# Kernel tuning notes

Hardware: AMD Instinct MI355X
Metric: run time of the kernel (lower is better)

## Reference

```python
import jax, jax.numpy as jnp
import numpy as np

H, W = 256, 256
FRONT_K = 8
ALPHA_T = 1.0 / 255.0
EPS = 1e-8               # transmittance early-stop threshold (meta_f32[4])
BG = (0.0, 0.0, 0.0)     # background color
CHUNK = 128              # gaussians composited per scan step


def setup_inputs() -> dict:
    key = jax.random.key(0)
    k1, k2, k3, k4, k5, k6, k7 = jax.random.split(key, 7)
    B, G = 2, 8192
    # gaussian centers spread over the image plane
    means2d = jax.random.uniform(k1, (B, G, 2), jnp.float32) * jnp.array([W, H], jnp.float32)
    # positive-definite conics (inverse 2D covariance): a, c > 0, |b| < sqrt(a*c)
    a = 0.05 + 0.45 * jax.random.uniform(k2, (B, G), jnp.float32)
    c = 0.05 + 0.45 * jax.random.uniform(k3, (B, G), jnp.float32)
    b = 0.5 * (jax.random.uniform(k4, (B, G), jnp.float32) - 0.5) * jnp.sqrt(a * c)
    conics = jnp.stack([a, b, c], axis=-1)
    colors = jax.random.uniform(k5, (B, G, 3), jnp.float32)
    opacities = jax.random.uniform(k6, (B, G), jnp.float32)
    depths = jax.random.uniform(k7, (B, G), jnp.float32) * 10.0
    return {"means2d": means2d, "conics": conics, "colors": colors,
            "opacities": opacities, "depths": depths}


def _rasterize_one(means2d, conics, colors, opacities, depths):
    # depth sort (stable, front-to-back)
    perm = jnp.argsort(depths, stable=True)
    m = means2d[perm]      # [G,2]
    co = conics[perm]      # [G,3]
    col = colors[perm]     # [G,3]
    op = opacities[perm]   # [G]
    G = m.shape[0]
    n_chunks = G // CHUNK

    px = jnp.arange(W, dtype=jnp.float32) + 0.5  # pixel centers
    py = jnp.arange(H, dtype=jnp.float32) + 0.5
    bg = jnp.asarray(BG, jnp.float32)

    def step(carry, chunk):
        accum, T, count = carry                    # [H,W,3], [H,W], [H,W] int32
        mC, coC, colC, opC = chunk                 # [K,2],[K,3],[K,3],[K]
        dx = px[None, None, :] - mC[:, 0][:, None, None]   # [K,1,W]
        dy = py[None, :, None] - mC[:, 1][:, None, None]   # [K,H,1]
        a = coC[:, 0][:, None, None]
        b = coC[:, 1][:, None, None]
        c = coC[:, 2][:, None, None]
        sigma = 0.5 * (a * dx * dx + c * dy * dy) + b * dx * dy  # [K,H,W]
        alpha = jnp.minimum(opC[:, None, None] * jnp.exp(-sigma), 0.999)
        alpha = jnp.where((sigma >= 0.0) & (alpha >= ALPHA_T), alpha, 0.0)
        kept = (alpha > 0.0).astype(jnp.int32)
        # front_k: only the first FRONT_K contributing gaussians per pixel
        before = count[None] + jnp.cumsum(kept, axis=0) - kept
        alpha = jnp.where(before < FRONT_K, alpha, 0.0)
        kept = (alpha > 0.0).astype(jnp.int32)
        one_m = 1.0 - alpha
        cp = jnp.cumprod(one_m, axis=0)                              # [K,H,W]
        Tc = T[None] * jnp.concatenate([jnp.ones((1, H, W), alpha.dtype), cp[:-1]], 0)
        w = jnp.where(Tc > EPS, Tc * alpha, 0.0)                     # early-stop gate
        accum = accum + jnp.einsum('khw,kc->hwc', w, colC)
        T = T * cp[-1]
        count = count + jnp.sum(kept, axis=0)
        return (accum, T, count), None

    chunks = (m.reshape(n_chunks, CHUNK, 2),
              co.reshape(n_chunks, CHUNK, 3),
              col.reshape(n_chunks, CHUNK, 3),
              op.reshape(n_chunks, CHUNK))
    init = (jnp.zeros((H, W, 3), jnp.float32),
            jnp.ones((H, W), jnp.float32),
            jnp.zeros((H, W), jnp.int32))
    (accum, T, _), _ = jax.lax.scan(step, init, chunks)
    return accum + T[..., None] * bg


def reference(means2d, conics, colors, opacities, depths):
    return jax.vmap(_rasterize_one)(means2d, conics, colors, opacities, depths)
```

## Files before the change

### kernel.cpp

```cpp
#include <hip/hip_runtime.h>
#include <math.h>

#define GN 8192
#define BN 2
#define HN 256
#define WN 256
#define FRONT_K 8
#define EPS_T 1e-8f
#define ALPHA_T (1.0f / 255.0f)
#define TDIM 32
#define NTILE (TDIM * TDIM)
#define CAP 256

__global__ __launch_bounds__(64) void pgr_clear(unsigned* __restrict__ cur)
{
    cur[blockIdx.x * 64 + threadIdx.x] = 0u;
}

__global__ __launch_bounds__(64) void pgr_prep(
    const float* __restrict__ means2d, const float* __restrict__ conics,
    const float* __restrict__ colors, const float* __restrict__ opac,
    float4* __restrict__ dat0, float4* __restrict__ dat1,
    float* __restrict__ dat2, unsigned* __restrict__ cur,
    unsigned* __restrict__ ent)
{
    int g = blockIdx.x * 64 + threadIdx.x;
    int b = g >> 13, i = g & (GN - 1);
    float2 mxy = reinterpret_cast<const float2*>(means2d)[g];
    float mx = mxy.x, my = mxy.y;
    float ca = conics[3 * g], cb = conics[3 * g + 1], cc = conics[3 * g + 2];
    float r = colors[3 * g], g2 = colors[3 * g + 1], b3 = colors[3 * g + 2];
    float op = opac[g];

    dat0[g] = make_float4(mx, my, ca, cb);
    dat1[g] = make_float4(cc, op, r, g2);
    dat2[g] = b3;

    float s = (op > 0.f) ? (__logf(255.0f * op) + 1e-4f) : -1.0f;
    if (s < 0.f) return;
    float det = fmaxf(ca * cc - cb * cb, 1e-12f);
    float dxm = sqrtf(2.f * s * cc / det) + 0.02f;
    float dym = sqrtf(2.f * s * ca / det) + 0.02f;
    int x0 = (int)floorf(mx - dxm - 0.5f), x1 = (int)ceilf(mx + dxm - 0.5f);
    int y0 = (int)floorf(my - dym - 0.5f), y1 = (int)ceilf(my + dym - 0.5f);
    if (x1 < 0 || x0 > WN - 1 || y1 < 0 || y0 > HN - 1) return;
    x0 = max(x0, 0); x1 = min(x1, WN - 1);
    y0 = max(y0, 0); y1 = min(y1, HN - 1);
    int tx0 = x0 >> 3, tx1 = x1 >> 3, ty0 = y0 >> 3, ty1 = y1 >> 3;
    for (int ty = ty0; ty <= ty1; ++ty)
        for (int tx = tx0; tx <= tx1; ++tx) {
            int t = b * NTILE + ty * TDIM + tx;
            unsigned pos = atomicAdd(&cur[t], 1u);
            if (pos < CAP) ent[t * CAP + pos] = (unsigned)i;
        }
}

__device__ __forceinline__ int rank_of(const unsigned long long* s_key,
                                       unsigned long long k, int L)
{
    int rank = 0, j = 0;
    for (; j + 4 <= L; j += 4) {
        unsigned long long k0 = s_key[j], k1 = s_key[j + 1];
        unsigned long long k2 = s_key[j + 2], k3 = s_key[j + 3];
        rank += (int)(k0 < k) + (int)(k1 < k) + (int)(k2 < k) + (int)(k3 < k);
    }
    for (; j < L; ++j) rank += (int)(s_key[j] < k);
    return rank;
}

__global__ __launch_bounds__(64) void pgr_raster(
    const float* __restrict__ depths, const float4* __restrict__ dat0,
    const float4* __restrict__ dat1, const float* __restrict__ dat2,
    const unsigned* __restrict__ cur, const unsigned* __restrict__ ent,
    float* __restrict__ out)
{
    const int b = blockIdx.z;
    const int t = b * NTILE + blockIdx.y * TDIM + blockIdx.x;
    const int tid = threadIdx.x;
    const int tx0 = blockIdx.x * 8, ty0 = blockIdx.y * 8;
    const int lx = tid & 7, ly = tid >> 3;
    const float px = tx0 + lx + 0.5f, py = ty0 + ly + 0.5f;
    const int bG = b * GN;

    __shared__ unsigned long long s_key[CAP];
    __shared__ float4 s_d0[CAP], s_d1[CAP];
    __shared__ float s_d2[CAP];

    unsigned eRaw = ent[t * CAP + tid];
    int e = (int)(eRaw & (GN - 1));
    int q = bG + e;
    float myd = depths[q];
    float4 r0 = dat0[q];
    float4 r1 = dat1[q];
    float r2 = dat2[q];
    const int L = min((int)cur[t], CAP);

    unsigned long long myk =
        ((unsigned long long)__float_as_uint(myd) << 13) | (unsigned)e;
    if (tid < L) s_key[tid] = myk;
    for (int i = 64 + tid; i < L; i += 64) {
        int ei = (int)(ent[t * CAP + i] & (GN - 1));
        s_key[i] = ((unsigned long long)__float_as_uint(depths[bG + ei]) << 13)
                   | (unsigned)ei;
    }
    __syncthreads();

    if (tid < L) {
        int rank = rank_of(s_key, myk, L);
        s_d0[rank] = r0; s_d1[rank] = r1; s_d2[rank] = r2;
    }
    for (int i = 64 + tid; i < L; i += 64) {
        unsigned long long k = s_key[i];
        int rank = rank_of(s_key, k, L);
        int qq = bG + (int)(k & (GN - 1));
        s_d0[rank] = dat0[qq]; s_d1[rank] = dat1[qq]; s_d2[rank] = dat2[qq];
    }
    __syncthreads();

    float accR = 0.f, accG = 0.f, accB = 0.f, T = 1.f;
    int count = 0;
    bool done = false;

    for (int i0 = 0; i0 < L; i0 += 8) {
        if (__all((int)done)) break;
        float alpha[8], colR[8], colG[8], colB[8];
        bool valid[8];
        #pragma unroll
        for (int k = 0; k < 8; ++k) {
            int idx = i0 + k;
            bool act = (idx < L) && !done;
            int ii = act ? idx : i0;
            float4 d0 = s_d0[ii];
            float4 d1 = s_d1[ii];
            float dx = __fsub_rn(px, d0.x);
            float dy = __fsub_rn(py, d0.y);
            float t1 = __fmul_rn(__fmul_rn(d0.z, dx), dx);
            float t2 = __fmul_rn(__fmul_rn(d1.x, dy), dy);
            float sigma = __fadd_rn(__fmul_rn(0.5f, __fadd_rn(t1, t2)),
                                    __fmul_rn(__fmul_rn(d0.w, dx), dy));
            bool v = act && sigma >= 0.f && sigma <= 5.55f;
            float al = v ? fminf(__fmul_rn(d1.y, __expf(-sigma)), 0.999f) : 0.f;
            valid[k] = v && (al >= ALPHA_T);
            alpha[k] = al;
            colR[k] = d1.z; colG[k] = d1.w; colB[k] = s_d2[ii];
        }
        #pragma unroll
        for (int k = 0; k < 8; ++k) {
            if (valid[k] && !done) {
                float al = alpha[k];
                if (T > EPS_T) {
                    float w = __fmul_rn(T, al);
                    accR += w * colR[k];
                    accG += w * colG[k];
                    accB += w * colB[k];
                }
                T = __fmul_rn(T, __fsub_rn(1.f, al));
                count++;
                if (count >= FRONT_K || T <= EPS_T) done = true;
            }
        }
    }

    int o = ((b * HN + (ty0 + ly)) * WN + (tx0 + lx)) * 3;
    out[o] = accR;
    out[o + 1] = accG;
    out[o + 2] = accB;
}

extern "C" void kernel_launch(void* const* d_in, const int* in_sizes, int n_in,
                              void* d_out, int out_size, void* d_ws, size_t ws_size,
                              hipStream_t stream) {
    const float* means2d = (const float*)d_in[0];
    const float* conics  = (const float*)d_in[1];
    const float* colors  = (const float*)d_in[2];
    const float* opac    = (const float*)d_in[3];
    const float* depths  = (const float*)d_in[4];
    float* out = (float*)d_out;

    const int BG = BN * GN;
    float4*   dat0 = (float4*)d_ws;
    float4*   dat1 = dat0 + BG;
    float*    dat2 = (float*)(dat1 + BG);
    unsigned* cur  = (unsigned*)(dat2 + BG);
    unsigned* ent  = cur + BN * NTILE;

    pgr_clear<<<(BN * NTILE) / 64, 64, 0, stream>>>(cur);
    pgr_prep<<<BG / 64, 64, 0, stream>>>(means2d, conics, colors, opac,
                                         dat0, dat1, dat2, cur, ent);
    pgr_raster<<<dim3(TDIM, TDIM, BN), 64, 0, stream>>>(
        depths, dat0, dat1, dat2, cur, ent, out);
}
```

Measured before the change: 46.70 us.

## Scatter full gaussian records and sort keys into per-tile bins during prep

The prep kernel now writes the depth key and all gaussian attributes (float4 x2 plus blue) directly into each tile's bin slot, instead of writing only the index and storing attributes once per gaussian. The raster kernel then reads keys and records contiguously per tile, with no indirect gathers through the index into depths and the attribute arrays. The cost is much more write traffic in prep (about 40 bytes per tile overlap instead of 4) and a far larger workspace footprint.

```diff
diff --git a/kernel.cpp b/kernel.cpp
--- a/kernel.cpp
+++ b/kernel.cpp
@@ -20,9 +20,10 @@
 __global__ __launch_bounds__(64) void pgr_prep(
     const float* __restrict__ means2d, const float* __restrict__ conics,
     const float* __restrict__ colors, const float* __restrict__ opac,
-    float4* __restrict__ dat0, float4* __restrict__ dat1,
-    float* __restrict__ dat2, unsigned* __restrict__ cur,
-    unsigned* __restrict__ ent)
+    const float* __restrict__ depths,
+    unsigned* __restrict__ cur, unsigned long long* __restrict__ kent,
+    float4* __restrict__ recA, float4* __restrict__ recB,
+    float* __restrict__ recC)
 {
     int g = blockIdx.x * 64 + threadIdx.x;
     int b = g >> 13, i = g & (GN - 1);
@@ -31,10 +32,7 @@
     float ca = conics[3 * g], cb = conics[3 * g + 1], cc = conics[3 * g + 2];
     float r = colors[3 * g], g2 = colors[3 * g + 1], b3 = colors[3 * g + 2];
     float op = opac[g];
-
-    dat0[g] = make_float4(mx, my, ca, cb);
-    dat1[g] = make_float4(cc, op, r, g2);
-    dat2[g] = b3;
+    float dep = depths[g];
 
     float s = (op > 0.f) ? (__logf(255.0f * op) + 1e-4f) : -1.0f;
     if (s < 0.f) return;
@@ -47,11 +45,23 @@
     x0 = max(x0, 0); x1 = min(x1, WN - 1);
     y0 = max(y0, 0); y1 = min(y1, HN - 1);
     int tx0 = x0 >> 3, tx1 = x1 >> 3, ty0 = y0 >> 3, ty1 = y1 >> 3;
+
+    unsigned long long key =
+        ((unsigned long long)__float_as_uint(dep) << 13) | (unsigned)i;
+    float4 A = make_float4(mx, my, ca, cb);
+    float4 B = make_float4(cc, op, r, g2);
+
     for (int ty = ty0; ty <= ty1; ++ty)
         for (int tx = tx0; tx <= tx1; ++tx) {
             int t = b * NTILE + ty * TDIM + tx;
             unsigned pos = atomicAdd(&cur[t], 1u);
-            if (pos < CAP) ent[t * CAP + pos] = (unsigned)i;
+            if (pos < CAP) {
+                int sl = t * CAP + (int)pos;
+                kent[sl] = key;
+                recA[sl] = A;
+                recB[sl] = B;
+                recC[sl] = b3;
+            }
         }
 }
 
@@ -69,10 +79,9 @@
 }
 
 __global__ __launch_bounds__(64) void pgr_raster(
-    const float* __restrict__ depths, const float4* __restrict__ dat0,
-    const float4* __restrict__ dat1, const float* __restrict__ dat2,
-    const unsigned* __restrict__ cur, const unsigned* __restrict__ ent,
-    float* __restrict__ out)
+    const unsigned* __restrict__ cur, const unsigned long long* __restrict__ kent,
+    const float4* __restrict__ recA, const float4* __restrict__ recB,
+    const float* __restrict__ recC, float* __restrict__ out)
 {
     const int b = blockIdx.z;
     const int t = b * NTILE + blockIdx.y * TDIM + blockIdx.x;
@@ -80,29 +89,21 @@
     const int tx0 = blockIdx.x * 8, ty0 = blockIdx.y * 8;
     const int lx = tid & 7, ly = tid >> 3;
     const float px = tx0 + lx + 0.5f, py = ty0 + ly + 0.5f;
-    const int bG = b * GN;
 
     __shared__ unsigned long long s_key[CAP];
     __shared__ float4 s_d0[CAP], s_d1[CAP];
     __shared__ float s_d2[CAP];
 
-    unsigned eRaw = ent[t * CAP + tid];
-    int e = (int)(eRaw & (GN - 1));
-    int q = bG + e;
-    float myd = depths[q];
-    float4 r0 = dat0[q];
-    float4 r1 = dat1[q];
-    float r2 = dat2[q];
+    const int base = t * CAP;
+    unsigned long long myk = kent[base + tid];
+    float4 r0 = recA[base + tid];
+    float4 r1 = recB[base + tid];
+    float r2 = recC[base + tid];
     const int L = min((int)cur[t], CAP);
 
-    unsigned long long myk =
-        ((unsigned long long)__float_as_uint(myd) << 13) | (unsigned)e;
     if (tid < L) s_key[tid] = myk;
-    for (int i = 64 + tid; i < L; i += 64) {
-        int ei = (int)(ent[t * CAP + i] & (GN - 1));
-        s_key[i] = ((unsigned long long)__float_as_uint(depths[bG + ei]) << 13)
-                   | (unsigned)ei;
-    }
+    for (int i = 64 + tid; i < L; i += 64)
+        s_key[i] = kent[base + i];
     __syncthreads();
 
     if (tid < L) {
@@ -110,10 +111,10 @@
         s_d0[rank] = r0; s_d1[rank] = r1; s_d2[rank] = r2;
     }
     for (int i = 64 + tid; i < L; i += 64) {
-        unsigned long long k = s_key[i];
-        int rank = rank_of(s_key, k, L);
-        int qq = bG + (int)(k & (GN - 1));
-        s_d0[rank] = dat0[qq]; s_d1[rank] = dat1[qq]; s_d2[rank] = dat2[qq];
+        int rank = rank_of(s_key, s_key[i], L);
+        s_d0[rank] = recA[base + i];
+        s_d1[rank] = recB[base + i];
+        s_d2[rank] = recC[base + i];
     }
     __syncthreads();
 
@@ -177,16 +178,16 @@
     const float* depths  = (const float*)d_in[4];
     float* out = (float*)d_out;
 
-    const int BG = BN * GN;
-    float4*   dat0 = (float4*)d_ws;
-    float4*   dat1 = dat0 + BG;
-    float*    dat2 = (float*)(dat1 + BG);
-    unsigned* cur  = (unsigned*)(dat2 + BG);
-    unsigned* ent  = cur + BN * NTILE;
+    const int NSLOT = BN * NTILE * CAP;
+    float4*             recA = (float4*)d_ws;
+    float4*             recB = recA + NSLOT;
+    unsigned long long* kent = (unsigned long long*)(recB + NSLOT);
+    float*              recC = (float*)(kent + NSLOT);
+    unsigned*           cur  = (unsigned*)(recC + NSLOT);
 
     pgr_clear<<<(BN * NTILE) / 64, 64, 0, stream>>>(cur);
-    pgr_prep<<<BG / 64, 64, 0, stream>>>(means2d, conics, colors, opac,
-                                         dat0, dat1, dat2, cur, ent);
+    pgr_prep<<<(BN * GN) / 64, 64, 0, stream>>>(means2d, conics, colors, opac,
+                                                depths, cur, kent, recA, recB, recC);
     pgr_raster<<<dim3(TDIM, TDIM, BN), 64, 0, stream>>>(
-        depths, dat0, dat1, dat2, cur, ent, out);
+        cur, kent, recA, recB, recC, out);
 }
```

New measurement: 47.91 us. +2.6%, slower.
